# Kernel tuning notes

Hardware: AMD Instinct MI355X
Metric: run time of the kernel (lower is better)

The kernel has to match this reference:

```python
import jax, jax.numpy as jnp
import numpy as np

N_NODES = 50000
N_GRAPHS = 512


def gcn_conv(x, W, b, row, col, norm, n_nodes):
    # PyG GCNConv: h = x @ W; out_i = sum_{j->i} norm_ij * h_j + b
    h = x @ W  # [N, H]
    msgs = h[row] * norm[:, None]  # gather source features, scale
    out = jax.ops.segment_sum(msgs, col, num_segments=n_nodes)
    return out + b


def reference(x, edge_index, batch, W0, b0, W1, b1, W2, b2, Wf, bf):
    n = x.shape[0]
    src, dst = edge_index[0], edge_index[1]
    # add self loops
    loop = jnp.arange(n)
    row = jnp.concatenate([src, loop])
    col = jnp.concatenate([dst, loop])
    # symmetric degree normalization: 1/sqrt(deg_i * deg_j)
    deg = jax.ops.segment_sum(jnp.ones_like(col, dtype=x.dtype), col, num_segments=n)
    dis = jnp.where(deg > 0, 1.0 / jnp.sqrt(deg), 0.0)
    norm = dis[row] * dis[col]

    h = x
    for W, b in ((W0, b0), (W1, b1), (W2, b2)):
        h = jax.nn.relu(gcn_conv(h, W, b, row, col, norm, n))
        # dropout is identity in eval mode

    # global mean pool over graphs
    sums = jax.ops.segment_sum(h, batch, num_segments=N_GRAPHS)
    counts = jax.ops.segment_sum(jnp.ones((n,), dtype=h.dtype), batch, num_segments=N_GRAPHS)
    pooled = sums / jnp.maximum(counts, 1.0)[:, None]  # [B, H]

    logits = pooled @ Wf + bf
    return jax.nn.log_softmax(logits, axis=1)


def setup_inputs() -> dict:
    key = jax.random.key(0)
    ks = jax.random.split(key, 12)
    d_in, d_h, d_out = 128, 128, 10
    x = jax.random.normal(ks[0], (N_NODES, d_in), dtype=jnp.float32)
    edge_index = jax.random.randint(ks[1], (2, 600000), 0, N_NODES, dtype=jnp.int64)
    batch = jnp.sort(jax.random.randint(ks[2], (N_NODES,), 0, N_GRAPHS, dtype=jnp.int64))
    s = 1.0 / np.sqrt(d_h)
    return {
        "x": x,
        "edge_index": edge_index,
        "batch": batch,
        "W0": jax.random.normal(ks[3], (d_in, d_h), dtype=jnp.float32) * s,
        "b0": jnp.zeros((d_h,), dtype=jnp.float32),
        "W1": jax.random.normal(ks[4], (d_h, d_h), dtype=jnp.float32) * s,
        "b1": jnp.zeros((d_h,), dtype=jnp.float32),
        "W2": jax.random.normal(ks[5], (d_h, d_h), dtype=jnp.float32) * s,
        "b2": jnp.zeros((d_h,), dtype=jnp.float32),
        "Wf": jax.random.normal(ks[6], (d_h, d_out), dtype=jnp.float32) * s,
        "bf": jnp.zeros((d_out,), dtype=jnp.float32),
    }
```

## Files before the change

kernel.cpp:

```cpp
#include <hip/hip_runtime.h>
#include <hip/hip_bf16.h>

#define NN 50000
#define NE 600000
#define NG 512

typedef __attribute__((ext_vector_type(8))) short bf16x8;
typedef __attribute__((ext_vector_type(4))) float f32x4;

__device__ __forceinline__ float bf_lo(unsigned u) {
    unsigned v = u << 16;
    return __builtin_bit_cast(float, v);
}
__device__ __forceinline__ float bf_hi(unsigned u) {
    unsigned v = u & 0xFFFF0000u;
    return __builtin_bit_cast(float, v);
}
__device__ __forceinline__ unsigned f2bf(float f) {
    unsigned u = __builtin_bit_cast(unsigned, f);
    return (u + 0x7FFFu + ((u >> 16) & 1u)) >> 16;
}

__global__ __launch_bounds__(256) void k_zero(float* p, int n) {
    int i = blockIdx.x * 256 + threadIdx.x;
    if (i < n) p[i] = 0.0f;
}

__global__ __launch_bounds__(256) void k_hist(const int* __restrict__ dst, int* __restrict__ deg) {
    int e = blockIdx.x * 256 + threadIdx.x;
    if (e < NE) atomicAdd(&deg[dst[e]], 1);
}

__global__ __launch_bounds__(256) void k_counts(const int* __restrict__ batch, float* __restrict__ counts) {
    int i = blockIdx.x * 256 + threadIdx.x;
    if (i < NN) atomicAdd(&counts[batch[i]], 1.0f);
}

__global__ __launch_bounds__(256) void k_alloc(const int* __restrict__ deg, int* __restrict__ gcur,
                                               int* __restrict__ rowstart, int* __restrict__ cursor,
                                               float* __restrict__ dis) {
    int i = blockIdx.x * 256 + threadIdx.x;
    if (i >= NN) return;
    int d = deg[i];
    int st = atomicAdd(gcur, d);
    rowstart[i] = st;
    cursor[i] = st;
    dis[i] = 1.0f / sqrtf((float)(d + 1));
}

__global__ __launch_bounds__(256) void k_fill(const int* __restrict__ src, const int* __restrict__ dst,
                                              const float* __restrict__ dis, int* __restrict__ cursor,
                                              int* __restrict__ csrc, float* __restrict__ cw) {
    int e = blockIdx.x * 256 + threadIdx.x;
    if (e >= NE) return;
    int s = src[e], d = dst[e];
    int slot = atomicAdd(&cursor[d], 1);
    csrc[slot] = s;
    cw[slot] = dis[s] * dis[d];
}

__global__ __launch_bounds__(256) void k_cvt_x(const float4* __restrict__ in, uint2* __restrict__ out, int n4) {
    int i = blockIdx.x * 256 + threadIdx.x;
    if (i >= n4) return;
    float4 v = in[i];
    uint2 o;
    o.x = f2bf(v.x) | (f2bf(v.y) << 16);
    o.y = f2bf(v.z) | (f2bf(v.w) << 16);
    out[i] = o;
}

__global__ __launch_bounds__(256) void k_cvt_w(const float* __restrict__ W0, const float* __restrict__ W1,
                                               const float* __restrict__ W2, unsigned short* __restrict__ Wt) {
    int idx = blockIdx.x * 256 + threadIdx.x;
    if (idx >= 3 * 16384) return;
    int m = idx >> 14;
    int r = idx & 16383;
    int k = r >> 7, c = r & 127;
    const float* W = (m == 0) ? W0 : (m == 1) ? W1 : W2;
    Wt[m * 16384 + c * 128 + k] = (unsigned short)f2bf(W[k * 128 + c]);
}

__global__ __launch_bounds__(256) void k_gemm_mfma(const unsigned short* __restrict__ A,
                                                   const unsigned short* __restrict__ Wt,
                                                   unsigned short* __restrict__ C, int M) {
    int wave = threadIdx.x >> 6;
    int lane = threadIdx.x & 63;
    int rowbase = blockIdx.x * 64 + wave * 16;
    int lr = lane & 15;
    int kg = lane >> 4;

    int arow = rowbase + lr;
    if (arow >= M) arow = M - 1;
    bf16x8 a[4];
#pragma unroll
    for (int kt = 0; kt < 4; ++kt)
        a[kt] = *(const bf16x8*)&A[arow * 128 + kt * 32 + kg * 8];

    f32x4 acc[8];
#pragma unroll
    for (int nt = 0; nt < 8; ++nt) acc[nt] = (f32x4){0.f, 0.f, 0.f, 0.f};

#pragma unroll
    for (int nt = 0; nt < 8; ++nt) {
        const unsigned short* wp = &Wt[(nt * 16 + lr) * 128 + kg * 8];
#pragma unroll
        for (int kt = 0; kt < 4; ++kt) {
            bf16x8 b = *(const bf16x8*)&wp[kt * 32];
            acc[nt] = __builtin_amdgcn_mfma_f32_16x16x32_bf16(a[kt], b, acc[nt], 0, 0, 0);
        }
    }

    int crow0 = rowbase + (lane >> 4) * 4;
#pragma unroll
    for (int nt = 0; nt < 8; ++nt) {
#pragma unroll
        for (int r = 0; r < 4; ++r) {
            int gr = crow0 + r;
            if (gr < M) C[gr * 128 + nt * 16 + lr] = (unsigned short)f2bf(acc[nt][r]);
        }
    }
}

template <int POOL>
__global__ __launch_bounds__(256) void k_gather(const uint2* __restrict__ h,
                                                const int* __restrict__ rowstart,
                                                const int* __restrict__ rowend,
                                                const int* __restrict__ csrc,
                                                const float* __restrict__ cw,
                                                const float* __restrict__ dis,
                                                const float* __restrict__ bias,
                                                uint2* __restrict__ outbuf,
                                                const int* __restrict__ batch,
                                                float* __restrict__ sums) {
    int t = blockIdx.x * 256 + threadIdx.x;
    int node = t >> 5;
    if (node >= NN) return;
    int f = t & 31;

    float d = dis[node];
    float w0 = d * d;
    uint2 hv = h[node * 32 + f];
    float a0 = bf_lo(hv.x) * w0;
    float a1 = bf_hi(hv.x) * w0;
    float a2 = bf_lo(hv.y) * w0;
    float a3 = bf_hi(hv.y) * w0;

    int s = rowstart[node];
    int e = rowend[node];
    for (; s < e; ++s) {
        int sn = csrc[s];
        float w = cw[s];
        uint2 v = h[sn * 32 + f];
        a0 = fmaf(bf_lo(v.x), w, a0);
        a1 = fmaf(bf_hi(v.x), w, a1);
        a2 = fmaf(bf_lo(v.y), w, a2);
        a3 = fmaf(bf_hi(v.y), w, a3);
    }

    float4 b = ((const float4*)bias)[f];
    a0 = fmaxf(a0 + b.x, 0.f);
    a1 = fmaxf(a1 + b.y, 0.f);
    a2 = fmaxf(a2 + b.z, 0.f);
    a3 = fmaxf(a3 + b.w, 0.f);

    if (POOL == 0) {
        uint2 o;
        o.x = f2bf(a0) | (f2bf(a1) << 16);
        o.y = f2bf(a2) | (f2bf(a3) << 16);
        outbuf[node * 32 + f] = o;
    } else {
        int g = batch[node];
        float* o = sums + g * 128 + f * 4;
        atomicAdd(o + 0, a0);
        atomicAdd(o + 1, a1);
        atomicAdd(o + 2, a2);
        atomicAdd(o + 3, a3);
    }
}

__global__ __launch_bounds__(64) void k_head(const float* __restrict__ sums,
                                             const float* __restrict__ counts,
                                             const float* __restrict__ Wf,
                                             const float* __restrict__ bf,
                                             float* __restrict__ out) {
    int g = blockIdx.x;
    int l = threadIdx.x;
    float inv = 1.0f / fmaxf(counts[g], 1.0f);
    float p0 = sums[g * 128 + l] * inv;
    float p1 = sums[g * 128 + 64 + l] * inv;
    float logit[10];
#pragma unroll
    for (int o = 0; o < 10; ++o) {
        float part = p0 * Wf[l * 10 + o] + p1 * Wf[(l + 64) * 10 + o];
#pragma unroll
        for (int s = 32; s > 0; s >>= 1) part += __shfl_xor(part, s);
        logit[o] = part + bf[o];
    }
    if (l == 0) {
        float m = logit[0];
#pragma unroll
        for (int o = 1; o < 10; ++o) m = fmaxf(m, logit[o]);
        float sum = 0.f;
#pragma unroll
        for (int o = 0; o < 10; ++o) sum += expf(logit[o] - m);
        float lse = m + logf(sum);
#pragma unroll
        for (int o = 0; o < 10; ++o) out[g * 10 + o] = logit[o] - lse;
    }
}

extern "C" void kernel_launch(void* const* d_in, const int* in_sizes, int n_in,
                              void* d_out, int out_size, void* d_ws, size_t ws_size,
                              hipStream_t stream) {
    const float* x     = (const float*)d_in[0];
    const int*   ei    = (const int*)d_in[1];
    const int*   batch = (const int*)d_in[2];
    const float* W0 = (const float*)d_in[3];
    const float* b0 = (const float*)d_in[4];
    const float* W1 = (const float*)d_in[5];
    const float* b1 = (const float*)d_in[6];
    const float* W2 = (const float*)d_in[7];
    const float* b2 = (const float*)d_in[8];
    const float* Wf = (const float*)d_in[9];
    const float* bf = (const float*)d_in[10];
    float* out = (float*)d_out;

    float* ws = (float*)d_ws;
    float* sums    = ws;
    float* counts  = ws + 65536;
    int*   in_deg  = (int*)(ws + 66048);
    int*   gcur    = (int*)(ws + 116096);
    float* dis     = ws + 116160;
    int*   rowstart= (int*)(ws + 166208);
    int*   cursor  = (int*)(ws + 216256);
    int*   csr_src = (int*)(ws + 266304);
    float* csr_w   = ws + 866368;
    unsigned short* Wt = (unsigned short*)(ws + 1466432);
    unsigned short* bx = (unsigned short*)(ws + 1491008);
    unsigned short* hA = (unsigned short*)(ws + 4691008);
    unsigned short* hB = (unsigned short*)(ws + 7891008);

    const int* src = ei;
    const int* dst = ei + NE;

    k_zero<<<(116160 + 255) / 256, 256, 0, stream>>>(ws, 116160);
    k_hist<<<2344, 256, 0, stream>>>(dst, in_deg);
    k_counts<<<196, 256, 0, stream>>>(batch, counts);
    k_alloc<<<196, 256, 0, stream>>>(in_deg, gcur, rowstart, cursor, dis);
    k_fill<<<2344, 256, 0, stream>>>(src, dst, dis, cursor, csr_src, csr_w);
    k_cvt_x<<<6250, 256, 0, stream>>>((const float4*)x, (uint2*)bx, NN * 32);
    k_cvt_w<<<192, 256, 0, stream>>>(W0, W1, W2, Wt);

    const int GEMM_GRID = (NN + 63) / 64;

    k_gemm_mfma<<<GEMM_GRID, 256, 0, stream>>>(bx, Wt, hB, NN);
    k_gather<0><<<6250, 256, 0, stream>>>((const uint2*)hB, rowstart, cursor, csr_src, csr_w,
                                          dis, b0, (uint2*)hA, batch, sums);
    k_gemm_mfma<<<GEMM_GRID, 256, 0, stream>>>(hA, Wt + 16384, hB, NN);
    k_gather<0><<<6250, 256, 0, stream>>>((const uint2*)hB, rowstart, cursor, csr_src, csr_w,
                                          dis, b1, (uint2*)hA, batch, sums);
    k_gemm_mfma<<<GEMM_GRID, 256, 0, stream>>>(hA, Wt + 32768, hB, NN);
    k_gather<1><<<6250, 256, 0, stream>>>((const uint2*)hB, rowstart, cursor, csr_src, csr_w,
                                          dis, b2, nullptr, batch, sums);

    k_head<<<512, 64, 0, stream>>>(sums, counts, Wf, bf, out);
}
```

Measured before the change: 408.2 us.

## Split each node's edge list across four lane groups with 16-byte loads in gather

The gather kernel now gives one 64-lane wavefront per node instead of 32 lanes. The wavefront is split into four groups of 16 lanes, and each group processes a different subset of the neighbor edges. Each lane loads 8 bf16 features as a uint4, and two edges per group are in flight each iteration. Partial sums are combined with cross-lane shuffles. The aim is more memory-level parallelism on the average ~13-edge rows and wider loads. In exchange it doubles the thread count, adds shuffle-reduction overhead, and leaves 3/4 of lanes idle on the store/atomic phase.

New measurement: 482.9 us. +18.3%, slower.

```diff
diff --git a/kernel.cpp b/kernel.cpp
--- a/kernel.cpp
+++ b/kernel.cpp
@@ -122,59 +122,102 @@
 }
 
 template <int POOL>
-__global__ __launch_bounds__(256) void k_gather(const uint2* __restrict__ h,
+__global__ __launch_bounds__(256) void k_gather(const uint4* __restrict__ h,
                                                 const int* __restrict__ rowstart,
                                                 const int* __restrict__ rowend,
                                                 const int* __restrict__ csrc,
                                                 const float* __restrict__ cw,
                                                 const float* __restrict__ dis,
                                                 const float* __restrict__ bias,
-                                                uint2* __restrict__ outbuf,
+                                                uint4* __restrict__ outbuf,
                                                 const int* __restrict__ batch,
                                                 float* __restrict__ sums) {
-    int t = blockIdx.x * 256 + threadIdx.x;
-    int node = t >> 5;
+    int node = (blockIdx.x * 256 + threadIdx.x) >> 6;
     if (node >= NN) return;
-    int f = t & 31;
+    int lane = threadIdx.x & 63;
+    int g = lane >> 4;
+    int sl = lane & 15;
+
+    int s0 = rowstart[node];
+    int e0 = rowend[node];
+
+    float a[8];
+#pragma unroll
+    for (int j = 0; j < 8; ++j) a[j] = 0.f;
+
+    for (int i = s0; i < e0; i += 8) {
+        int ia = i + g;
+        int ib = i + 4 + g;
+        bool oka = ia < e0;
+        bool okb = ib < e0;
+        int sa = oka ? ia : s0;
+        int sb = okb ? ib : s0;
+        int sna = csrc[sa];
+        int snb = csrc[sb];
+        float wa = oka ? cw[sa] : 0.f;
+        float wb = okb ? cw[sb] : 0.f;
+        uint4 va = h[sna * 16 + sl];
+        uint4 vb = h[snb * 16 + sl];
+        a[0] = fmaf(bf_lo(va.x), wa, a[0]);
+        a[1] = fmaf(bf_hi(va.x), wa, a[1]);
+        a[2] = fmaf(bf_lo(va.y), wa, a[2]);
+        a[3] = fmaf(bf_hi(va.y), wa, a[3]);
+        a[4] = fmaf(bf_lo(va.z), wa, a[4]);
+        a[5] = fmaf(bf_hi(va.z), wa, a[5]);
+        a[6] = fmaf(bf_lo(va.w), wa, a[6]);
+        a[7] = fmaf(bf_hi(va.w), wa, a[7]);
+        a[0] = fmaf(bf_lo(vb.x), wb, a[0]);
+        a[1] = fmaf(bf_hi(vb.x), wb, a[1]);
+        a[2] = fmaf(bf_lo(vb.y), wb, a[2]);
+        a[3] = fmaf(bf_hi(vb.y), wb, a[3]);
+        a[4] = fmaf(bf_lo(vb.z), wb, a[4]);
+        a[5] = fmaf(bf_hi(vb.z), wb, a[5]);
+        a[6] = fmaf(bf_lo(vb.w), wb, a[6]);
+        a[7] = fmaf(bf_hi(vb.w), wb, a[7]);
+    }
+
+#pragma unroll
+    for (int j = 0; j < 8; ++j) {
+        a[j] += __shfl_xor(a[j], 16);
+        a[j] += __shfl_xor(a[j], 32);
+    }
 
     float d = dis[node];
     float w0 = d * d;
-    uint2 hv = h[node * 32 + f];
-    float a0 = bf_lo(hv.x) * w0;
-    float a1 = bf_hi(hv.x) * w0;
-    float a2 = bf_lo(hv.y) * w0;
-    float a3 = bf_hi(hv.y) * w0;
-
-    int s = rowstart[node];
-    int e = rowend[node];
-    for (; s < e; ++s) {
-        int sn = csrc[s];
-        float w = cw[s];
-        uint2 v = h[sn * 32 + f];
-        a0 = fmaf(bf_lo(v.x), w, a0);
-        a1 = fmaf(bf_hi(v.x), w, a1);
-        a2 = fmaf(bf_lo(v.y), w, a2);
-        a3 = fmaf(bf_hi(v.y), w, a3);
-    }
-
-    float4 b = ((const float4*)bias)[f];
-    a0 = fmaxf(a0 + b.x, 0.f);
-    a1 = fmaxf(a1 + b.y, 0.f);
-    a2 = fmaxf(a2 + b.z, 0.f);
-    a3 = fmaxf(a3 + b.w, 0.f);
-
-    if (POOL == 0) {
-        uint2 o;
-        o.x = f2bf(a0) | (f2bf(a1) << 16);
-        o.y = f2bf(a2) | (f2bf(a3) << 16);
-        outbuf[node * 32 + f] = o;
-    } else {
-        int g = batch[node];
-        float* o = sums + g * 128 + f * 4;
-        atomicAdd(o + 0, a0);
-        atomicAdd(o + 1, a1);
-        atomicAdd(o + 2, a2);
-        atomicAdd(o + 3, a3);
+    uint4 hv = h[node * 16 + sl];
+    a[0] = fmaf(bf_lo(hv.x), w0, a[0]);
+    a[1] = fmaf(bf_hi(hv.x), w0, a[1]);
+    a[2] = fmaf(bf_lo(hv.y), w0, a[2]);
+    a[3] = fmaf(bf_hi(hv.y), w0, a[3]);
+    a[4] = fmaf(bf_lo(hv.z), w0, a[4]);
+    a[5] = fmaf(bf_hi(hv.z), w0, a[5]);
+    a[6] = fmaf(bf_lo(hv.w), w0, a[6]);
+    a[7] = fmaf(bf_hi(hv.w), w0, a[7]);
+    float4 ba = ((const float4*)bias)[sl * 2];
+    float4 bb = ((const float4*)bias)[sl * 2 + 1];
+    a[0] = fmaxf(a[0] + ba.x, 0.f);
+    a[1] = fmaxf(a[1] + ba.y, 0.f);
+    a[2] = fmaxf(a[2] + ba.z, 0.f);
+    a[3] = fmaxf(a[3] + ba.w, 0.f);
+    a[4] = fmaxf(a[4] + bb.x, 0.f);
+    a[5] = fmaxf(a[5] + bb.y, 0.f);
+    a[6] = fmaxf(a[6] + bb.z, 0.f);
+    a[7] = fmaxf(a[7] + bb.w, 0.f);
+
+    if (g == 0) {
+        if (POOL == 0) {
+            uint4 o;
+            o.x = f2bf(a[0]) | (f2bf(a[1]) << 16);
+            o.y = f2bf(a[2]) | (f2bf(a[3]) << 16);
+            o.z = f2bf(a[4]) | (f2bf(a[5]) << 16);
+            o.w = f2bf(a[6]) | (f2bf(a[7]) << 16);
+            outbuf[node * 16 + sl] = o;
+        } else {
+            int gg = batch[node];
+            float* o = sums + gg * 128 + sl * 8;
+#pragma unroll
+            for (int j = 0; j < 8; ++j) atomicAdd(o + j, a[j]);
+        }
     }
 }
 
@@ -252,16 +295,17 @@
     k_cvt_w<<<192, 256, 0, stream>>>(W0, W1, W2, Wt);
 
     const int GEMM_GRID = (NN + 63) / 64;
+    const int GATHER_GRID = (NN * 64 + 255) / 256;
 
     k_gemm_mfma<<<GEMM_GRID, 256, 0, stream>>>(bx, Wt, hB, NN);
-    k_gather<0><<<6250, 256, 0, stream>>>((const uint2*)hB, rowstart, cursor, csr_src, csr_w,
-                                          dis, b0, (uint2*)hA, batch, sums);
+    k_gather<0><<<GATHER_GRID, 256, 0, stream>>>((const uint4*)hB, rowstart, cursor, csr_src, csr_w,
+                                                 dis, b0, (uint4*)hA, batch, sums);
     k_gemm_mfma<<<GEMM_GRID, 256, 0, stream>>>(hA, Wt + 16384, hB, NN);
-    k_gather<0><<<6250, 256, 0, stream>>>((const uint2*)hB, rowstart, cursor, csr_src, csr_w,
-                                          dis, b1, (uint2*)hA, batch, sums);
+    k_gather<0><<<GATHER_GRID, 256, 0, stream>>>((const uint4*)hB, rowstart, cursor, csr_src, csr_w,
+                                                 dis, b1, (uint4*)hA, batch, sums);
     k_gemm_mfma<<<GEMM_GRID, 256, 0, stream>>>(hA, Wt + 32768, hB, NN);
-    k_gather<1><<<6250, 256, 0, stream>>>((const uint2*)hB, rowstart, cursor, csr_src, csr_w,
-                                          dis, b2, nullptr, batch, sums);
+    k_gather<1><<<GATHER_GRID, 256, 0, stream>>>((const uint4*)hB, rowstart, cursor, csr_src, csr_w,
+                                                 dis, b2, nullptr, batch, sums);
 
     k_head<<<512, 64, 0, stream>>>(sums, counts, Wf, bf, out);
 }
```

## Pack CSR source and weight, pad rows to 4, unroll gather loop

Applied to the files above, without the earlier changes.

The CSR source index and edge weight now live in one interleaved uint2 array instead of two separate arrays. Each row's start is padded to a multiple of 4, and the padding slots hold zero entries (source 0, weight 0). This lets the gather loop load four edges with two 16-byte loads and issue four independent feature gathers into separate accumulators, which is meant to raise memory-level parallelism and cut index-load instructions. In exchange, rows do a little extra work on padded entries that read node 0's features, and the CSR buffer grows.

Result: faster. 363.4 us, median of 2 (-11.0%).

```diff
diff --git a/kernel.cpp b/kernel.cpp
--- a/kernel.cpp
+++ b/kernel.cpp
@@ -38,25 +38,26 @@
 
 __global__ __launch_bounds__(256) void k_alloc(const int* __restrict__ deg, int* __restrict__ gcur,
                                                int* __restrict__ rowstart, int* __restrict__ cursor,
-                                               float* __restrict__ dis) {
+                                               float* __restrict__ dis, uint2* __restrict__ cpk) {
     int i = blockIdx.x * 256 + threadIdx.x;
     if (i >= NN) return;
     int d = deg[i];
-    int st = atomicAdd(gcur, d);
+    int dr = (d + 3) & ~3;
+    int st = atomicAdd(gcur, dr);
     rowstart[i] = st;
     cursor[i] = st;
     dis[i] = 1.0f / sqrtf((float)(d + 1));
+    for (int p = st + d; p < st + dr; ++p) cpk[p] = make_uint2(0u, 0u);
 }
 
 __global__ __launch_bounds__(256) void k_fill(const int* __restrict__ src, const int* __restrict__ dst,
                                               const float* __restrict__ dis, int* __restrict__ cursor,
-                                              int* __restrict__ csrc, float* __restrict__ cw) {
+                                              uint2* __restrict__ cpk) {
     int e = blockIdx.x * 256 + threadIdx.x;
     if (e >= NE) return;
     int s = src[e], d = dst[e];
     int slot = atomicAdd(&cursor[d], 1);
-    csrc[slot] = s;
-    cw[slot] = dis[s] * dis[d];
+    cpk[slot] = make_uint2((unsigned)s, __builtin_bit_cast(unsigned, dis[s] * dis[d]));
 }
 
 __global__ __launch_bounds__(256) void k_cvt_x(const float4* __restrict__ in, uint2* __restrict__ out, int n4) {
@@ -125,8 +126,7 @@
 __global__ __launch_bounds__(256) void k_gather(const uint2* __restrict__ h,
                                                 const int* __restrict__ rowstart,
                                                 const int* __restrict__ rowend,
-                                                const int* __restrict__ csrc,
-                                                const float* __restrict__ cw,
+                                                const uint2* __restrict__ cpk,
                                                 const float* __restrict__ dis,
                                                 const float* __restrict__ bias,
                                                 uint2* __restrict__ outbuf,
@@ -137,25 +137,55 @@
     if (node >= NN) return;
     int f = t & 31;
 
+    int s0 = rowstart[node];
+    int e0 = rowend[node];
+
+    float A0 = 0.f, A1 = 0.f, A2 = 0.f, A3 = 0.f;
+    float B0 = 0.f, B1 = 0.f, B2 = 0.f, B3 = 0.f;
+    float C0 = 0.f, C1 = 0.f, C2 = 0.f, C3 = 0.f;
+    float D0 = 0.f, D1 = 0.f, D2 = 0.f, D3 = 0.f;
+
+    for (int s = s0; s < e0; s += 4) {
+        uint4 q01 = *(const uint4*)&cpk[s];
+        uint4 q23 = *(const uint4*)&cpk[s + 2];
+        uint2 v0 = h[(int)q01.x * 32 + f];
+        uint2 v1 = h[(int)q01.z * 32 + f];
+        uint2 v2 = h[(int)q23.x * 32 + f];
+        uint2 v3 = h[(int)q23.z * 32 + f];
+        float w0 = __builtin_bit_cast(float, q01.y);
+        float w1 = __builtin_bit_cast(float, q01.w);
+        float w2 = __builtin_bit_cast(float, q23.y);
+        float w3 = __builtin_bit_cast(float, q23.w);
+        A0 = fmaf(bf_lo(v0.x), w0, A0);
+        A1 = fmaf(bf_hi(v0.x), w0, A1);
+        A2 = fmaf(bf_lo(v0.y), w0, A2);
+        A3 = fmaf(bf_hi(v0.y), w0, A3);
+        B0 = fmaf(bf_lo(v1.x), w1, B0);
+        B1 = fmaf(bf_hi(v1.x), w1, B1);
+        B2 = fmaf(bf_lo(v1.y), w1, B2);
+        B3 = fmaf(bf_hi(v1.y), w1, B3);
+        C0 = fmaf(bf_lo(v2.x), w2, C0);
+        C1 = fmaf(bf_hi(v2.x), w2, C1);
+        C2 = fmaf(bf_lo(v2.y), w2, C2);
+        C3 = fmaf(bf_hi(v2.y), w2, C3);
+        D0 = fmaf(bf_lo(v3.x), w3, D0);
+        D1 = fmaf(bf_hi(v3.x), w3, D1);
+        D2 = fmaf(bf_lo(v3.y), w3, D2);
+        D3 = fmaf(bf_hi(v3.y), w3, D3);
+    }
+
     float d = dis[node];
     float w0 = d * d;
     uint2 hv = h[node * 32 + f];
-    float a0 = bf_lo(hv.x) * w0;
-    float a1 = bf_hi(hv.x) * w0;
-    float a2 = bf_lo(hv.y) * w0;
-    float a3 = bf_hi(hv.y) * w0;
-
-    int s = rowstart[node];
-    int e = rowend[node];
-    for (; s < e; ++s) {
-        int sn = csrc[s];
-        float w = cw[s];
-        uint2 v = h[sn * 32 + f];
-        a0 = fmaf(bf_lo(v.x), w, a0);
-        a1 = fmaf(bf_hi(v.x), w, a1);
-        a2 = fmaf(bf_lo(v.y), w, a2);
-        a3 = fmaf(bf_hi(v.y), w, a3);
-    }
+    A0 = fmaf(bf_lo(hv.x), w0, A0);
+    A1 = fmaf(bf_hi(hv.x), w0, A1);
+    A2 = fmaf(bf_lo(hv.y), w0, A2);
+    A3 = fmaf(bf_hi(hv.y), w0, A3);
+
+    float a0 = (A0 + B0) + (C0 + D0);
+    float a1 = (A1 + B1) + (C1 + D1);
+    float a2 = (A2 + B2) + (C2 + D2);
+    float a3 = (A3 + B3) + (C3 + D3);
 
     float4 b = ((const float4*)bias)[f];
     a0 = fmaxf(a0 + b.x, 0.f);
@@ -233,12 +263,11 @@
     float* dis     = ws + 116160;
     int*   rowstart= (int*)(ws + 166208);
     int*   cursor  = (int*)(ws + 216256);
-    int*   csr_src = (int*)(ws + 266304);
-    float* csr_w   = ws + 866368;
-    unsigned short* Wt = (unsigned short*)(ws + 1466432);
-    unsigned short* bx = (unsigned short*)(ws + 1491008);
-    unsigned short* hA = (unsigned short*)(ws + 4691008);
-    unsigned short* hB = (unsigned short*)(ws + 7891008);
+    uint2* cpk     = (uint2*)(ws + 266304);
+    unsigned short* Wt = (unsigned short*)(ws + 1866432);
+    unsigned short* bx = (unsigned short*)(ws + 1891008);
+    unsigned short* hA = (unsigned short*)(ws + 5091008);
+    unsigned short* hB = (unsigned short*)(ws + 8291008);
 
     const int* src = ei;
     const int* dst = ei + NE;
@@ -246,21 +275,21 @@
     k_zero<<<(116160 + 255) / 256, 256, 0, stream>>>(ws, 116160);
     k_hist<<<2344, 256, 0, stream>>>(dst, in_deg);
     k_counts<<<196, 256, 0, stream>>>(batch, counts);
-    k_alloc<<<196, 256, 0, stream>>>(in_deg, gcur, rowstart, cursor, dis);
-    k_fill<<<2344, 256, 0, stream>>>(src, dst, dis, cursor, csr_src, csr_w);
+    k_alloc<<<196, 256, 0, stream>>>(in_deg, gcur, rowstart, cursor, dis, cpk);
+    k_fill<<<2344, 256, 0, stream>>>(src, dst, dis, cursor, cpk);
     k_cvt_x<<<6250, 256, 0, stream>>>((const float4*)x, (uint2*)bx, NN * 32);
     k_cvt_w<<<192, 256, 0, stream>>>(W0, W1, W2, Wt);
 
     const int GEMM_GRID = (NN + 63) / 64;
 
     k_gemm_mfma<<<GEMM_GRID, 256, 0, stream>>>(bx, Wt, hB, NN);
-    k_gather<0><<<6250, 256, 0, stream>>>((const uint2*)hB, rowstart, cursor, csr_src, csr_w,
+    k_gather<0><<<6250, 256, 0, stream>>>((const uint2*)hB, rowstart, cursor, cpk,
                                           dis, b0, (uint2*)hA, batch, sums);
     k_gemm_mfma<<<GEMM_GRID, 256, 0, stream>>>(hA, Wt + 16384, hB, NN);
-    k_gather<0><<<6250, 256, 0, stream>>>((const uint2*)hB, rowstart, cursor, csr_src, csr_w,
+    k_gather<0><<<6250, 256, 0, stream>>>((const uint2*)hB, rowstart, cursor, cpk,
                                           dis, b1, (uint2*)hA, batch, sums);
     k_gemm_mfma<<<GEMM_GRID, 256, 0, stream>>>(hA, Wt + 32768, hB, NN);
-    k_gather<1><<<6250, 256, 0, stream>>>((const uint2*)hB, rowstart, cursor, csr_src, csr_w,
+    k_gather<1><<<6250, 256, 0, stream>>>((const uint2*)hB, rowstart, cursor, cpk,
                                           dis, b2, nullptr, batch, sums);
 
     k_head<<<512, 64, 0, stream>>>(sums, counts, Wf, bf, out);
```
